# Kernel tuning notes

Hardware: AMD Instinct MI355X
Metric: run time of the kernel (lower is better)

## Reference

```python
import jax, jax.numpy as jnp
import numpy as np

B, L, DIM, H = 2, 2048, 1024, 16
HD = DIM // H  # head dim = 64
MASK_SCALE = -10 * 6  # faithful to the original source: mask_expand *= -10 * 6


def setup_inputs() -> dict:
    key = jax.random.key(0)
    ks = jax.random.split(key, 8)
    s = 1.0 / np.sqrt(DIM)
    return {
        "x": jax.random.normal(ks[0], (B, L, DIM), jnp.float32),
        "attention_mask": jax.random.uniform(ks[1], (B, L, L), jnp.float32),
        "Wq": jax.random.normal(ks[2], (DIM, DIM), jnp.float32) * s,
        "bq": jnp.zeros((DIM,), jnp.float32),
        "Wk": jax.random.normal(ks[3], (DIM, DIM), jnp.float32) * s,
        "bk": jnp.zeros((DIM,), jnp.float32),
        "Wv": jax.random.normal(ks[4], (DIM, DIM), jnp.float32) * s,
        "bv": jnp.zeros((DIM,), jnp.float32),
    }


def _split_heads(t):
    # [B, L, DIM] -> [B, H, L, HD]
    return t.reshape(B, L, H, HD).transpose(0, 2, 1, 3)


def reference(x, attention_mask, Wq, bq, Wk, bk, Wv, bv):
    q = _split_heads(x @ Wq + bq)
    k = _split_heads(x @ Wk + bk)
    v = _split_heads(x @ Wv + bv)
    scale = float(HD) ** -0.5
    # full [B, H, L, L] score matrix, as in the original
    scores = jnp.einsum("bhqd,bhkd->bhqk", q, k) * scale
    scores = scores + attention_mask[:, None, :, :] * MASK_SCALE
    probs = jax.nn.softmax(scores, axis=-1)
    ctx = jnp.einsum("bhqk,bhkd->bhqd", probs, v)
    # merge heads back: [B, L, DIM]
    return ctx.transpose(0, 2, 1, 3).reshape(B, L, DIM)
```

## Files before the change

kernel.cpp:

```cpp
#include <hip/hip_runtime.h>

#define LL 2048
#define NHEADS 16
#define HDIM 64
#define QSCALE 0.18033688011112042f
#define MASKC1 -86.56170245333780f

typedef __attribute__((ext_vector_type(8))) __bf16 bf16x8;
typedef __attribute__((ext_vector_type(4))) float f32x4;
typedef __attribute__((ext_vector_type(4))) unsigned int u32x4;

__device__ __forceinline__ unsigned short f2bf(float f) {
  unsigned int u = __builtin_bit_cast(unsigned int, f);
  u += 0x7fffu + ((u >> 16) & 1u);
  return (unsigned short)(u >> 16);
}

__device__ __forceinline__ bf16x8 ld_frag(const unsigned short* p) {
  return *reinterpret_cast<const bf16x8*>(p);
}

__device__ __forceinline__ float bflo(unsigned int u) {
  return __builtin_bit_cast(float, u << 16);
}
__device__ __forceinline__ float bfhi(unsigned int u) {
  return __builtin_bit_cast(float, u & 0xffff0000u);
}
__device__ __forceinline__ unsigned int pack2(float hi, float lo) {
  return __builtin_amdgcn_perm(__builtin_bit_cast(unsigned int, hi),
                               __builtin_bit_cast(unsigned int, lo), 0x07060302u);
}

__device__ __forceinline__ void async_cp16(const unsigned short* g, unsigned short* l) {
  __builtin_amdgcn_global_load_lds(
      (const __attribute__((address_space(1))) unsigned int*)(unsigned long long)(g),
      (__attribute__((address_space(3))) unsigned int*)(unsigned int)(unsigned long long)(l),
      16, 0, 0);
}

__device__ __forceinline__ void lem_load(const unsigned short* p, uint4& a, uint4& b,
                                         uint4& c, uint4& d) {
  asm volatile("global_load_dwordx4 %0, %4, off\n\t"
               "global_load_dwordx4 %1, %4, off offset:16\n\t"
               "global_load_dwordx4 %2, %4, off offset:32\n\t"
               "global_load_dwordx4 %3, %4, off offset:48"
               : "=&v"(a), "=&v"(b), "=&v"(c), "=&v"(d)
               : "v"(p)
               : "memory");
}

__global__ __launch_bounds__(256) void prep_kernel(const float* __restrict__ x,
                                                   const float* __restrict__ Wq,
                                                   const float* __restrict__ Wk,
                                                   const float* __restrict__ Wv,
                                                   unsigned short* __restrict__ xb,
                                                   unsigned short* __restrict__ WtAll) {
  const int z = blockIdx.z;
  if (z == 3) {
    const int bidx = blockIdx.y * 16 + blockIdx.x;
    const int base = bidx * 256 + threadIdx.x;
#pragma unroll
    for (int p = 0; p < 16; ++p) {
      int i = (p * 65536 + base) * 4;
      float4 v = *reinterpret_cast<const float4*>(x + i);
      ushort4 o;
      o.x = f2bf(v.x); o.y = f2bf(v.y); o.z = f2bf(v.z); o.w = f2bf(v.w);
      *reinterpret_cast<ushort4*>(xb + i) = o;
    }
    return;
  }
  const float* W = (z == 0) ? Wq : (z == 1) ? Wk : Wv;
  unsigned short* dst = WtAll + (size_t)z * 1024 * 1024;
  int n0 = blockIdx.x * 64, k0 = blockIdx.y * 64;
  __shared__ float t[64][65];
  int tx = threadIdx.x & 63, ty = threadIdx.x >> 6;
#pragma unroll
  for (int p = 0; p < 16; ++p) {
    int kr = p * 4 + ty;
    t[kr][tx] = W[(size_t)(k0 + kr) * 1024 + n0 + tx];
  }
  __syncthreads();
#pragma unroll
  for (int p = 0; p < 16; ++p) {
    int nr = p * 4 + ty;
    dst[(size_t)(n0 + nr) * 1024 + k0 + tx] = f2bf(t[tx][nr]);
  }
}

__global__ __launch_bounds__(256) void lem_prep_kernel(const float* __restrict__ mask,
                                                       unsigned short* __restrict__ lem) {
  const int qb = blockIdx.x, kt = blockIdx.y, b = blockIdx.z;
  const int tid = threadIdx.x;
  __shared__ unsigned short lds[128 * 72];
  {
    const int r0 = tid >> 4;
    const int c0 = (tid & 15) * 4;
#pragma unroll
    for (int p = 0; p < 8; ++p) {
      int row = p * 16 + r0;
      float4 v = *reinterpret_cast<const float4*>(
          mask + ((size_t)b * LL + qb * 128 + row) * LL + kt * 64 + c0);
      ushort4 o;
      o.x = f2bf(v.x * MASKC1); o.y = f2bf(v.y * MASKC1);
      o.z = f2bf(v.z * MASKC1); o.w = f2bf(v.w * MASKC1);
      *reinterpret_cast<ushort4*>(&lds[row * 72 + c0]) = o;
    }
  }
  __syncthreads();
  const int w = tid >> 6, lane = tid & 63, g = lane >> 4, cc = lane & 15;
  unsigned int ow[16];
#pragma unroll
  for (int mt = 0; mt < 2; ++mt) {
    const int q = w * 32 + mt * 16 + cc;
#pragma unroll
    for (int nt = 0; nt < 4; ++nt) {
      uint2 v = *reinterpret_cast<const uint2*>(&lds[q * 72 + nt * 16 + g * 4]);
      ow[mt * 8 + nt * 2]     = v.x;
      ow[mt * 8 + nt * 2 + 1] = v.y;
    }
  }
  uint4* dst = reinterpret_cast<uint4*>(
      lem + ((((size_t)b * 16 + qb) * 32 + kt) * 256 + tid) * 32);
#pragma unroll
  for (int j = 0; j < 4; ++j)
    dst[j] = make_uint4(ow[4 * j], ow[4 * j + 1], ow[4 * j + 2], ow[4 * j + 3]);
}

__global__ __launch_bounds__(256) void qkv_gemm_kernel(
    const unsigned short* __restrict__ xb, const unsigned short* __restrict__ WtAll,
    const float* __restrict__ bq, const float* __restrict__ bk, const float* __restrict__ bv,
    unsigned short* __restrict__ qkv) {
  const int z = blockIdx.z;
  const unsigned short* Wt = WtAll + (size_t)z * 1024 * 1024;
  const float* bias = (z == 0) ? bq : (z == 1) ? bk : bv;
  unsigned short* outb = qkv + (size_t)z * 4194304;

  __shared__ __align__(16) unsigned short smem[32768];

  const int tid = threadIdx.x;
  const int w = tid >> 6, lane = tid & 63, g = lane >> 4, cc = lane & 15;
  const int wm = w >> 1, wn = w & 1;
  const int m0 = blockIdx.y * 128, n0 = blockIdx.x * 128;
  const int srow = lane >> 3;
  const int gc = ((lane & 7) - srow) & 7;
  const unsigned short* ga = xb + (size_t)(m0 + w * 32 + srow) * 1024 + gc * 8;
  const unsigned short* gb = Wt + (size_t)(n0 + w * 32 + srow) * 1024 + gc * 8;

  f32x4 acc[4][4];
#pragma unroll
  for (int i = 0; i < 4; ++i)
#pragma unroll
    for (int j = 0; j < 4; ++j) acc[i][j] = (f32x4)0.0f;

#pragma unroll
  for (int i = 0; i < 4; ++i) {
    async_cp16(ga + i * 8192, smem + w * 2048 + i * 512);
    async_cp16(gb + i * 8192, smem + 8192 + w * 2048 + i * 512);
  }
#pragma unroll
  for (int i = 0; i < 4; ++i) {
    async_cp16(ga + i * 8192 + 64, smem + 16384 + w * 2048 + i * 512);
    async_cp16(gb + i * 8192 + 64, smem + 24576 + w * 2048 + i * 512);
  }

#define QITER(KT, BUF, VMC, ISSUE)                                                     \
  {                                                                                    \
    asm volatile("s_waitcnt vmcnt(" VMC ")" ::: "memory");                             \
    asm volatile("s_barrier" ::: "memory");                                            \
    {                                                                                  \
      const unsigned short* Ab = smem + (BUF) * 16384;                                 \
      const unsigned short* Bb = smem + (BUF) * 16384 + 8192;                          \
      bf16x8 af[4][2], bfr[4][2];                                                      \
      _Pragma("unroll") for (int mt = 0; mt < 4; ++mt)                                 \
        _Pragma("unroll") for (int ks = 0; ks < 2; ++ks)                               \
          af[mt][ks] =                                                                 \
              ld_frag(&Ab[(wm * 64 + mt * 16 + cc) * 64 + ((4 * ks + g + cc) & 7) * 8]);\
      _Pragma("unroll") for (int nt = 0; nt < 4; ++nt)                                 \
        _Pragma("unroll") for (int ks = 0; ks < 2; ++ks)                               \
          bfr[nt][ks] =                                                                \
              ld_frag(&Bb[(wn * 64 + nt * 16 + cc) * 64 + ((4 * ks + g + cc) & 7) * 8]);\
      __builtin_amdgcn_s_setprio(1);                                                   \
      _Pragma("unroll") for (int mt = 0; mt < 4; ++mt)                                 \
        _Pragma("unroll") for (int nt = 0; nt < 4; ++nt)                               \
          _Pragma("unroll") for (int ks = 0; ks < 2; ++ks)                             \
            acc[mt][nt] = __builtin_amdgcn_mfma_f32_16x16x32_bf16(af[mt][ks], bfr[nt][ks],\
                                                                  acc[mt][nt], 0, 0, 0);\
      __builtin_amdgcn_s_setprio(0);                                                   \
    }                                                                                  \
    asm volatile("s_barrier" ::: "memory");                                            \
    if (ISSUE) {                                                                       \
      _Pragma("unroll") for (int i = 0; i < 4; ++i) {                                  \
        async_cp16(ga + i * 8192 + ((KT) + 2) * 64, smem + (BUF) * 16384 + w * 2048 + i * 512);\
        async_cp16(gb + i * 8192 + ((KT) + 2) * 64,                                    \
                   smem + (BUF) * 16384 + 8192 + w * 2048 + i * 512);                  \
      }                                                                                \
    }                                                                                  \
  }

  for (int kt = 0; kt < 14; kt += 2) {
    QITER(kt + 0, 0, "8", true)
    QITER(kt + 1, 1, "8", true)
  }
  QITER(14, 0, "8", false)
  QITER(15, 1, "0", false)

#undef QITER

  if (z != 2) {
    const float sc = (z == 0) ? QSCALE : 1.0f;
#pragma unroll
    for (int nt = 0; nt < 4; ++nt) {
      int n = n0 + wn * 64 + nt * 16 + cc;
      float bval = bias[n];
      int h = n >> 6, d = n & 63;
#pragma unroll
      for (int mt = 0; mt < 4; ++mt) {
#pragma unroll
        for (int r = 0; r < 4; ++r) {
          int m = m0 + wm * 64 + mt * 16 + g * 4 + r;
          int b = m >> 11, l = m & 2047;
          outb[(((size_t)(b * NHEADS + h) * LL) + l) * HDIM + d] =
              f2bf((acc[mt][nt][r] + bval) * sc);
        }
      }
    }
  } else {
    __syncthreads();
#pragma unroll
    for (int nt = 0; nt < 4; ++nt) {
      int nr = wn * 64 + nt * 16 + cc;
      float bval = bias[n0 + nr];
#pragma unroll
      for (int mt = 0; mt < 4; ++mt)
#pragma unroll
        for (int r = 0; r < 4; ++r)
          smem[nr * 128 + wm * 64 + (mt >> 1) * 32 + g * 8 + (mt & 1) * 4 + r] =
              f2bf(acc[mt][nt][r] + bval);
    }
    __syncthreads();
    int row = tid >> 1, half = tid & 1;
    int n = n0 + row, hh = n >> 6, dd = n & 63;
    int bb = m0 >> 11, l0 = (m0 & 2047) + half * 64;
    unsigned short* dst = outb + ((size_t)(bb * NHEADS + hh) * HDIM + dd) * LL + l0;
#pragma unroll
    for (int i = 0; i < 8; ++i)
      *reinterpret_cast<uint4*>(dst + i * 8) =
          *reinterpret_cast<const uint4*>(&smem[row * 128 + half * 64 + i * 8]);
  }
}

__global__ __launch_bounds__(256, 2) void flash_kernel(
    const unsigned short* __restrict__ Qb, const unsigned short* __restrict__ Kb,
    const unsigned short* __restrict__ Vt, const unsigned short* __restrict__ Lem,
    float* __restrict__ out) {
  const int id = blockIdx.y * 16 + blockIdx.x;
  const int nid = (id & 7) * 64 + (id >> 3);
  const int qb = nid & 15, bh = nid >> 4;
  const int b = bh >> 4, h = bh & 15;
  const int q0 = qb * 128;
  const int tid = threadIdx.x, w = tid >> 6, lane = tid & 63, g = lane >> 4, cc = lane & 15;
  const size_t bhoff = (size_t)bh * LL * HDIM;

  __shared__ __align__(16) unsigned short Ks[3][64 * 64];
  __shared__ __align__(16) unsigned short Vs[3][64 * 64];

  bf16x8 aq[2][2];
#pragma unroll
  for (int mt = 0; mt < 2; ++mt)
#pragma unroll
    for (int ks = 0; ks < 2; ++ks)
      aq[mt][ks] = *reinterpret_cast<const bf16x8*>(
          Qb + bhoff + (size_t)(q0 + w * 32 + mt * 16 + cc) * HDIM + ks * 32 + g * 8);

  const int srow = lane >> 3;
  const int gcs = ((lane & 7) - srow) & 7;
  const unsigned short* kg0 = Kb + bhoff + (size_t)(w * 8 + srow) * HDIM + gcs * 8;
  const unsigned short* kg1 = Kb + bhoff + (size_t)(32 + w * 8 + srow) * HDIM + gcs * 8;
  const unsigned short* vg0 = Vt + bhoff + (size_t)(w * 8 + srow) * LL + gcs * 8;
  const unsigned short* vg1 = Vt + bhoff + (size_t)(32 + w * 8 + srow) * LL + gcs * 8;

  const unsigned short* lemq = Lem + (((size_t)b * 16 + qb) * 32 * 256 + tid) * 32;

  const u32x4 onesu = {0x3F803F80u, 0x3F803F80u, 0x3F803F80u, 0x3F803F80u};
  const bf16x8 bones = __builtin_bit_cast(bf16x8, onesu);

  uint4 l00, l01, l02, l03, l10, l11, l12, l13, l20, l21, l22, l23;

  f32x4 liacc[2];
  f32x4 oacc[2][4];
#pragma unroll
  for (int mt = 0; mt < 2; ++mt) {
    liacc[mt] = (f32x4)0.0f;
#pragma unroll
    for (int nt = 0; nt < 4; ++nt) oacc[mt][nt] = (f32x4)0.0f;
  }

  async_cp16(kg0, Ks[0] + w * 512);
  async_cp16(kg1, Ks[0] + (w + 4) * 512);
  async_cp16(vg0, Vs[0] + w * 512);
  async_cp16(vg1, Vs[0] + (w + 4) * 512);
  lem_load(lemq, l00, l01, l02, l03);
  lemq += 8192;
  async_cp16(kg0 + (size_t)64 * HDIM, Ks[1] + w * 512);
  async_cp16(kg1 + (size_t)64 * HDIM, Ks[1] + (w + 4) * 512);
  async_cp16(vg0 + 64, Vs[1] + w * 512);
  async_cp16(vg1 + 64, Vs[1] + (w + 4) * 512);
  lem_load(lemq, l10, l11, l12, l13);
  lemq += 8192;

#define FLASH_COMPUTE(BUF, LSA, LSB, LSC, LSD)                                         \
  {                                                                                    \
    bf16x8 bk_[4][2], bv[4][2];                                                        \
    _Pragma("unroll") for (int nt = 0; nt < 4; ++nt)                                   \
      _Pragma("unroll") for (int ks = 0; ks < 2; ++ks)                                 \
        bk_[nt][ks] =                                                                  \
            ld_frag(&Ks[BUF][(nt * 16 + cc) * 64 + ((4 * ks + g + cc) & 7) * 8]);      \
    _Pragma("unroll") for (int nt = 0; nt < 4; ++nt)                                   \
      _Pragma("unroll") for (int ks = 0; ks < 2; ++ks)                                 \
        bv[nt][ks] =                                                                   \
            ld_frag(&Vs[BUF][(nt * 16 + cc) * 64 + ((4 * ks + g + cc) & 7) * 8]);      \
    bf16x8 ap[2][2];                                                                   \
    _Pragma("unroll") for (int mt = 0; mt < 2; ++mt) {                                 \
      f32x4 sacc[4];                                                                   \
      const uint4 ea = (mt == 0) ? LSA : LSC;                                          \
      const uint4 eb = (mt == 0) ? LSB : LSD;                                          \
      sacc[0][0] = bflo(ea.x); sacc[0][1] = bfhi(ea.x);                                \
      sacc[0][2] = bflo(ea.y); sacc[0][3] = bfhi(ea.y);                                \
      sacc[1][0] = bflo(ea.z); sacc[1][1] = bfhi(ea.z);                                \
      sacc[1][2] = bflo(ea.w); sacc[1][3] = bfhi(ea.w);                                \
      sacc[2][0] = bflo(eb.x); sacc[2][1] = bfhi(eb.x);                                \
      sacc[2][2] = bflo(eb.y); sacc[2][3] = bfhi(eb.y);                                \
      sacc[3][0] = bflo(eb.z); sacc[3][1] = bfhi(eb.z);                                \
      sacc[3][2] = bflo(eb.w); sacc[3][3] = bfhi(eb.w);                                \
      __builtin_amdgcn_s_setprio(1);                                                   \
      _Pragma("unroll") for (int nt = 0; nt < 4; ++nt)                                 \
        _Pragma("unroll") for (int ks = 0; ks < 2; ++ks)                               \
          sacc[nt] = __builtin_amdgcn_mfma_f32_16x16x32_bf16(bk_[nt][ks], aq[mt][ks],  \
                                                             sacc[nt], 0, 0, 0);       \
      __builtin_amdgcn_s_setprio(0);                                                   \
      float p[4][4];                                                                   \
      _Pragma("unroll") for (int nt = 0; nt < 4; ++nt)                                 \
        _Pragma("unroll") for (int r = 0; r < 4; ++r)                                  \
          p[nt][r] = __builtin_amdgcn_exp2f(sacc[nt][r]);                              \
      unsigned int wd[8];                                                              \
      _Pragma("unroll") for (int ks = 0; ks < 2; ++ks) {                               \
        wd[ks * 4 + 0] = pack2(p[2 * ks][1],     p[2 * ks][0]);                        \
        wd[ks * 4 + 1] = pack2(p[2 * ks][3],     p[2 * ks][2]);                        \
        wd[ks * 4 + 2] = pack2(p[2 * ks + 1][1], p[2 * ks + 1][0]);                    \
        wd[ks * 4 + 3] = pack2(p[2 * ks + 1][3], p[2 * ks + 1][2]);                    \
        u32x4 uv = {wd[ks * 4], wd[ks * 4 + 1], wd[ks * 4 + 2], wd[ks * 4 + 3]};       \
        ap[mt][ks] = __builtin_bit_cast(bf16x8, uv);                                   \
      }                                                                                \
    }                                                                                  \
    __builtin_amdgcn_s_setprio(1);                                                     \
    _Pragma("unroll") for (int mt = 0; mt < 2; ++mt) {                                 \
      _Pragma("unroll") for (int nt = 0; nt < 4; ++nt)                                 \
        _Pragma("unroll") for (int ks = 0; ks < 2; ++ks)                               \
          oacc[mt][nt] = __builtin_amdgcn_mfma_f32_16x16x32_bf16(ap[mt][ks], bv[nt][ks],\
                                                                 oacc[mt][nt], 0, 0, 0);\
      _Pragma("unroll") for (int ks = 0; ks < 2; ++ks)                                 \
        liacc[mt] = __builtin_amdgcn_mfma_f32_16x16x32_bf16(ap[mt][ks], bones,         \
                                                            liacc[mt], 0, 0, 0);       \
    }                                                                                  \
    __builtin_amdgcn_s_setprio(0);                                                     \
  }

#define FITER(KT, CBUF, SBUF, VMC, ISSUE, UA, UB, UC, UD, LA, LB, LC, LD)              \
  {                                                                                    \
    asm volatile("s_waitcnt vmcnt(" VMC ")" ::: "memory");                             \
    __builtin_amdgcn_sched_barrier(0);                                                 \
    asm volatile("s_barrier" ::: "memory");                                            \
    __builtin_amdgcn_sched_barrier(0);                                                 \
    if (ISSUE) {                                                                       \
      const size_t ko = (size_t)((KT) + 2) * 64;                                       \
      async_cp16(kg0 + ko * HDIM, Ks[SBUF] + w * 512);                                 \
      async_cp16(kg1 + ko * HDIM, Ks[SBUF] + (w + 4) * 512);                           \
      async_cp16(vg0 + ko, Vs[SBUF] + w * 512);                                        \
      async_cp16(vg1 + ko, Vs[SBUF] + (w + 4) * 512);                                  \
      lem_load(lemq, LA, LB, LC, LD);                                                  \
      lemq += 8192;                                                                    \
    }                                                                                  \
    FLASH_COMPUTE(CBUF, UA, UB, UC, UD);                                               \
  }

  for (int kt = 0; kt < 30; kt += 3) {
    FITER(kt + 0, 0, 2, "8", true,  l00, l01, l02, l03, l20, l21, l22, l23)
    FITER(kt + 1, 1, 0, "8", true,  l10, l11, l12, l13, l00, l01, l02, l03)
    FITER(kt + 2, 2, 1, "8", true,  l20, l21, l22, l23, l10, l11, l12, l13)
  }
  FITER(30, 0, 0, "8", false, l00, l01, l02, l03, l00, l01, l02, l03)
  FITER(31, 1, 0, "0", false, l10, l11, l12, l13, l10, l11, l12, l13)

#undef FITER
#undef FLASH_COMPUTE

#pragma unroll
  for (int mt = 0; mt < 2; ++mt) {
#pragma unroll
    for (int r = 0; r < 4; ++r) {
      float inv = 1.0f / liacc[mt][r];
      int qrow = q0 + w * 32 + mt * 16 + g * 4 + r;
#pragma unroll
      for (int nt = 0; nt < 4; ++nt)
        out[((size_t)b * LL + qrow) * 1024 + h * 64 + nt * 16 + cc] = oacc[mt][nt][r] * inv;
    }
  }
}

extern "C" void kernel_launch(void* const* d_in, const int* in_sizes, int n_in,
                              void* d_out, int out_size, void* d_ws, size_t ws_size,
                              hipStream_t stream) {
  const float* x    = (const float*)d_in[0];
  const float* mask = (const float*)d_in[1];
  const float* Wq   = (const float*)d_in[2];
  const float* bq   = (const float*)d_in[3];
  const float* Wk   = (const float*)d_in[4];
  const float* bk   = (const float*)d_in[5];
  const float* Wv   = (const float*)d_in[6];
  const float* bv   = (const float*)d_in[7];
  float* out = (float*)d_out;
  (void)in_sizes; (void)n_in; (void)out_size; (void)ws_size;

  char* ws = (char*)d_ws;
  unsigned short* qkv = (unsigned short*)(ws);
  unsigned short* xb  = (unsigned short*)(ws + (24u << 20));
  unsigned short* Wt  = (unsigned short*)(ws + (32u << 20));
  unsigned short* lem = (unsigned short*)(ws + (24u << 20));

  prep_kernel<<<dim3(16, 16, 4), dim3(256), 0, stream>>>(x, Wq, Wk, Wv, xb, Wt);
  qkv_gemm_kernel<<<dim3(8, 32, 3), dim3(256), 0, stream>>>(xb, Wt, bq, bk, bv, qkv);
  lem_prep_kernel<<<dim3(16, 32, 2), dim3(256), 0, stream>>>(mask, lem);
  flash_kernel<<<dim3(16, 32), dim3(256), 0, stream>>>(qkv, qkv + 4194304, qkv + 8388608,
                                                       lem, out);
}
```

Measured before the change: 191.0 us.

## Process two KV tiles per barrier phase with double-buffered tile pairs

Restructures the flash-attention main loop from a triple-buffered one-tile-per-iteration pipeline into a double-buffered scheme where each phase stages and computes two 64-key tiles. Each phase waits on vmcnt(0) and takes one barrier per two tiles, halving barrier count. The cost is more LDS (4 tile slots instead of 3), more mask registers held in flight, and a full vmcnt drain each phase that may expose load latency, which could lower occupancy at 2 blocks/CU.

```diff
diff --git a/kernel.cpp b/kernel.cpp
--- a/kernel.cpp
+++ b/kernel.cpp
@@ -261,8 +261,8 @@
   const int tid = threadIdx.x, w = tid >> 6, lane = tid & 63, g = lane >> 4, cc = lane & 15;
   const size_t bhoff = (size_t)bh * LL * HDIM;
 
-  __shared__ __align__(16) unsigned short Ks[3][64 * 64];
-  __shared__ __align__(16) unsigned short Vs[3][64 * 64];
+  __shared__ __align__(16) unsigned short Ks[2][2][64 * 64];
+  __shared__ __align__(16) unsigned short Vs[2][2][64 * 64];
 
   bf16x8 aq[2][2];
 #pragma unroll
@@ -284,7 +284,8 @@
   const u32x4 onesu = {0x3F803F80u, 0x3F803F80u, 0x3F803F80u, 0x3F803F80u};
   const bf16x8 bones = __builtin_bit_cast(bf16x8, onesu);
 
-  uint4 l00, l01, l02, l03, l10, l11, l12, l13, l20, l21, l22, l23;
+  uint4 l00, l01, l02, l03, l10, l11, l12, l13;
+  uint4 l20, l21, l22, l23, l30, l31, l32, l33;
 
   f32x4 liacc[2];
   f32x4 oacc[2][4];
@@ -295,30 +296,32 @@
     for (int nt = 0; nt < 4; ++nt) oacc[mt][nt] = (f32x4)0.0f;
   }
 
-  async_cp16(kg0, Ks[0] + w * 512);
-  async_cp16(kg1, Ks[0] + (w + 4) * 512);
-  async_cp16(vg0, Vs[0] + w * 512);
-  async_cp16(vg1, Vs[0] + (w + 4) * 512);
+#define STAGE_KV(KT, BUF, TILE)                                                        \
+  {                                                                                    \
+    const size_t ko = (size_t)(KT) * 64;                                               \
+    async_cp16(kg0 + ko * HDIM, Ks[BUF][TILE] + w * 512);                              \
+    async_cp16(kg1 + ko * HDIM, Ks[BUF][TILE] + (w + 4) * 512);                        \
+    async_cp16(vg0 + ko, Vs[BUF][TILE] + w * 512);                                     \
+    async_cp16(vg1 + ko, Vs[BUF][TILE] + (w + 4) * 512);                               \
+  }
+
+  STAGE_KV(0, 0, 0)
+  STAGE_KV(1, 0, 1)
   lem_load(lemq, l00, l01, l02, l03);
-  lemq += 8192;
-  async_cp16(kg0 + (size_t)64 * HDIM, Ks[1] + w * 512);
-  async_cp16(kg1 + (size_t)64 * HDIM, Ks[1] + (w + 4) * 512);
-  async_cp16(vg0 + 64, Vs[1] + w * 512);
-  async_cp16(vg1 + 64, Vs[1] + (w + 4) * 512);
-  lem_load(lemq, l10, l11, l12, l13);
-  lemq += 8192;
-
-#define FLASH_COMPUTE(BUF, LSA, LSB, LSC, LSD)                                         \
+  lem_load(lemq + 8192, l10, l11, l12, l13);
+  lemq += 16384;
+
+#define FLASH_COMPUTE(BUF, TILE, LSA, LSB, LSC, LSD)                                   \
   {                                                                                    \
     bf16x8 bk_[4][2], bv[4][2];                                                        \
     _Pragma("unroll") for (int nt = 0; nt < 4; ++nt)                                   \
       _Pragma("unroll") for (int ks = 0; ks < 2; ++ks)                                 \
         bk_[nt][ks] =                                                                  \
-            ld_frag(&Ks[BUF][(nt * 16 + cc) * 64 + ((4 * ks + g + cc) & 7) * 8]);      \
+            ld_frag(&Ks[BUF][TILE][(nt * 16 + cc) * 64 + ((4 * ks + g + cc) & 7) * 8]);\
     _Pragma("unroll") for (int nt = 0; nt < 4; ++nt)                                   \
       _Pragma("unroll") for (int ks = 0; ks < 2; ++ks)                                 \
         bv[nt][ks] =                                                                   \
-            ld_frag(&Vs[BUF][(nt * 16 + cc) * 64 + ((4 * ks + g + cc) & 7) * 8]);      \
+            ld_frag(&Vs[BUF][TILE][(nt * 16 + cc) * 64 + ((4 * ks + g + cc) & 7) * 8]);\
     bf16x8 ap[2][2];                                                                   \
     _Pragma("unroll") for (int mt = 0; mt < 2; ++mt) {                                 \
       f32x4 sacc[4];                                                                   \
@@ -365,34 +368,37 @@
     __builtin_amdgcn_s_setprio(0);                                                     \
   }
 
-#define FITER(KT, CBUF, SBUF, VMC, ISSUE, UA, UB, UC, UD, LA, LB, LC, LD)              \
+#define PPHASE(P, CBUF, ISSUE, A0, A1, A2, A3, B0, B1, B2, B3, C0, C1, C2, C3, D0, D1, D2, D3) \
   {                                                                                    \
-    asm volatile("s_waitcnt vmcnt(" VMC ")" ::: "memory");                             \
+    asm volatile("s_waitcnt vmcnt(0)" ::: "memory");                                   \
     __builtin_amdgcn_sched_barrier(0);                                                 \
     asm volatile("s_barrier" ::: "memory");                                            \
     __builtin_amdgcn_sched_barrier(0);                                                 \
     if (ISSUE) {                                                                       \
-      const size_t ko = (size_t)((KT) + 2) * 64;                                       \
-      async_cp16(kg0 + ko * HDIM, Ks[SBUF] + w * 512);                                 \
-      async_cp16(kg1 + ko * HDIM, Ks[SBUF] + (w + 4) * 512);                           \
-      async_cp16(vg0 + ko, Vs[SBUF] + w * 512);                                        \
-      async_cp16(vg1 + ko, Vs[SBUF] + (w + 4) * 512);                                  \
-      lem_load(lemq, LA, LB, LC, LD);                                                  \
-      lemq += 8192;                                                                    \
+      STAGE_KV(2 * (P) + 2, (CBUF) ^ 1, 0)                                             \
+      STAGE_KV(2 * (P) + 3, (CBUF) ^ 1, 1)                                             \
+      lem_load(lemq, C0, C1, C2, C3);                                                  \
+      lem_load(lemq + 8192, D0, D1, D2, D3);                                           \
+      lemq += 16384;                                                                   \
     }                                                                                  \
-    FLASH_COMPUTE(CBUF, UA, UB, UC, UD);                                               \
-  }
-
-  for (int kt = 0; kt < 30; kt += 3) {
-    FITER(kt + 0, 0, 2, "8", true,  l00, l01, l02, l03, l20, l21, l22, l23)
-    FITER(kt + 1, 1, 0, "8", true,  l10, l11, l12, l13, l00, l01, l02, l03)
-    FITER(kt + 2, 2, 1, "8", true,  l20, l21, l22, l23, l10, l11, l12, l13)
-  }
-  FITER(30, 0, 0, "8", false, l00, l01, l02, l03, l00, l01, l02, l03)
-  FITER(31, 1, 0, "0", false, l10, l11, l12, l13, l10, l11, l12, l13)
-
-#undef FITER
+    FLASH_COMPUTE(CBUF, 0, A0, A1, A2, A3)                                             \
+    FLASH_COMPUTE(CBUF, 1, B0, B1, B2, B3)                                             \
+  }
+
+  for (int p = 0; p < 14; p += 2) {
+    PPHASE(p + 0, 0, true, l00, l01, l02, l03, l10, l11, l12, l13,
+                          l20, l21, l22, l23, l30, l31, l32, l33)
+    PPHASE(p + 1, 1, true, l20, l21, l22, l23, l30, l31, l32, l33,
+                          l00, l01, l02, l03, l10, l11, l12, l13)
+  }
+  PPHASE(14, 0, true,  l00, l01, l02, l03, l10, l11, l12, l13,
+                       l20, l21, l22, l23, l30, l31, l32, l33)
+  PPHASE(15, 1, false, l20, l21, l22, l23, l30, l31, l32, l33,
+                       l00, l01, l02, l03, l10, l11, l12, l13)
+
+#undef PPHASE
 #undef FLASH_COMPUTE
+#undef STAGE_KV
 
 #pragma unroll
   for (int mt = 0; mt < 2; ++mt) {
```

Measured after the change: 193.0 us. Within noise of the previous version (+1.0%).
